# Optimization experiments

Hardware: AMD Instinct MI355X
Metric: run time of the kernel (lower is better)

The kernel has to match this reference:

```python
import jax, jax.numpy as jnp
import numpy as np


def setup_inputs() -> dict:
    key = jax.random.key(0)
    k1, k2, k3 = jax.random.split(key, 3)
    N, D, E = 4096, 1024, 8  # tokens, d_model, path_num (experts)
    x = jax.random.normal(k1, (N, D), dtype=jnp.float32)
    score = jax.random.uniform(k2, (N, E), dtype=jnp.float32)
    hot_mask = jax.random.randint(k3, (N, E), 0, 2).astype(jnp.int32)
    tag = jnp.arange(N, dtype=jnp.int32).reshape(N, 1)
    return {"x": x, "score": score, "hot_mask": hot_mask, "tag": tag}


def reference(x, score, hot_mask, tag):
    # Per-expert gather dispatch with score scaling (route_logic='1d', transform=True).
    # Torch version produces variable-length per-expert flows; here each expert's
    # output is packed into a fixed capacity of N slots (selected tokens first,
    # in original order, matching torch.nonzero ordering), zero-padded beyond count.
    N, D = x.shape
    E = hot_mask.shape[1]
    mask = hot_mask > 0  # [N, E] multi-hot routing mask
    pos = jnp.arange(N)

    def dispatch(mask_e, score_e):
        # stable partition: selected tokens get their index, others index+N
        order = jnp.argsort(jnp.where(mask_e, pos, pos + N))  # [N]
        count = mask_e.sum()
        valid = pos < count  # [N] first `count` slots hold real tokens
        data = x * score_e[:, None]  # transform: scale by routing score
        out_data = jnp.where(valid[:, None], data[order], 0.0)  # [N, D]
        out_tag = jnp.where(valid[:, None], tag[order], 0)      # [N, 1]
        return out_data, out_tag, count

    out_data, out_tags, counts = jax.vmap(dispatch, in_axes=(1, 1))(mask, score)
    # out_data: [E, N, D], out_tags: [E, N, 1], counts: [E]
    return out_data, out_tags, counts
```

## Files before the change

kernel.cpp:

```cpp
#include <hip/hip_runtime.h>

#define N_TOK 4096
#define DMODEL 1024
#define NEXP 8
#define BT 256
#define TPB 16

__global__ __launch_bounds__(BT) void build(
        const int* __restrict__ hot_mask,
        int* __restrict__ perm,
        float* __restrict__ out_tags,
        float* __restrict__ out_cnts) {
    const int e = blockIdx.x;
    const int t = threadIdx.x;
    const int base = t * TPB;

    unsigned int bits = 0;
    int s = 0;
#pragma unroll
    for (int j = 0; j < TPB; ++j) {
        int m = (hot_mask[(size_t)(base + j) * NEXP + e] > 0) ? 1 : 0;
        bits |= (unsigned int)m << j;
        s += m;
    }

    __shared__ int sm[BT];
    sm[t] = s;
    __syncthreads();
    for (int off = 1; off < BT; off <<= 1) {
        int v = (t >= off) ? sm[t - off] : 0;
        __syncthreads();
        sm[t] += v;
        __syncthreads();
    }
    const int cnt = sm[BT - 1];
    int run = (t == 0) ? 0 : sm[t - 1];

#pragma unroll
    for (int j = 0; j < TPB; ++j) {
        if ((bits >> j) & 1u) {
            const int slot = run++;
            perm[e * N_TOK + slot] = base + j;
            out_tags[e * N_TOK + slot] = (float)(base + j);
        }
    }
    for (int slot = cnt + t; slot < N_TOK; slot += BT) {
        perm[e * N_TOK + slot] = -1;
        out_tags[e * N_TOK + slot] = 0.0f;
    }
    if (t == 0) out_cnts[e] = (float)cnt;
}

__global__ __launch_bounds__(256) void gather_f32(
        const float* __restrict__ x,
        const float* __restrict__ score,
        const int* __restrict__ perm,
        float* __restrict__ out_data)
{
    const int blk = blockIdx.x;
    const int t = threadIdx.x;
    const int n = perm[blk];
    float4* orow = reinterpret_cast<float4*>(out_data + (size_t)blk * DMODEL) + t;

    if (n >= 0) {
        const int e = blk >> 12;
        const int nn = n & (N_TOK - 1);
        const float sc = score[nn * NEXP + e];
        float4 v = reinterpret_cast<const float4*>(x + (size_t)nn * DMODEL)[t];
        v.x *= sc; v.y *= sc; v.z *= sc; v.w *= sc;
        *orow = v;
    } else {
        *orow = make_float4(0.f, 0.f, 0.f, 0.f);
    }
}

extern "C" void kernel_launch(void* const* d_in, const int* in_sizes, int n_in,
                              void* d_out, int out_size, void* d_ws, size_t ws_size,
                              hipStream_t stream) {
    const float* x        = (const float*)d_in[0];
    const float* score    = (const float*)d_in[1];
    const int*   hot_mask = (const int*)d_in[2];

    float* out      = (float*)d_out;
    float* out_data = out;
    float* out_tags = out + (size_t)NEXP * N_TOK * DMODEL;
    float* out_cnts = out_tags + (size_t)NEXP * N_TOK;

    int* perm = (int*)d_ws;

    build<<<NEXP, BT, 0, stream>>>(hot_mask, perm, out_tags, out_cnts);
    gather_f32<<<NEXP * N_TOK, 256, 0, stream>>>(x, score, perm, out_data);
}
```

Measured before the change: 38.63 us.

## Process 16 rows per gather block with nontemporal stores and shared perm/score

The gather kernel now uses 1024-thread blocks that each handle 16 output rows, with the permutation indices and routing scores loaded once into shared memory. Output is written with nontemporal stores so the 128 MB of output does not pollute the cache, and the build kernel moves to 512 threads with 8 tokens each. This cuts the block count and the per-row overhead of separate perm/score loads. It adds a block-wide barrier and a larger block size, which can reduce scheduling flexibility.

Result: faster. 36.38 us (-5.8%).

```diff
diff --git a/kernel.cpp b/kernel.cpp
--- a/kernel.cpp
+++ b/kernel.cpp
@@ -3,8 +3,11 @@
 #define N_TOK 4096
 #define DMODEL 1024
 #define NEXP 8
-#define BT 256
-#define TPB 16
+#define BT 512
+#define TPB 8
+#define RPB 16
+
+typedef float vfloat4 __attribute__((ext_vector_type(4)));
 
 __global__ __launch_bounds__(BT) void build(
         const int* __restrict__ hot_mask,
@@ -51,26 +54,43 @@
     if (t == 0) out_cnts[e] = (float)cnt;
 }
 
-__global__ __launch_bounds__(256) void gather_f32(
+__global__ __launch_bounds__(1024) void gather_f32(
         const float* __restrict__ x,
         const float* __restrict__ score,
         const int* __restrict__ perm,
         float* __restrict__ out_data)
 {
-    const int blk = blockIdx.x;
-    const int t = threadIdx.x;
-    const int n = perm[blk];
-    float4* orow = reinterpret_cast<float4*>(out_data + (size_t)blk * DMODEL) + t;
+    const int row0 = blockIdx.x * RPB;
+    const int e = row0 >> 12;
+    const int tid = threadIdx.x;
 
-    if (n >= 0) {
-        const int e = blk >> 12;
-        const int nn = n & (N_TOK - 1);
-        const float sc = score[nn * NEXP + e];
-        float4 v = reinterpret_cast<const float4*>(x + (size_t)nn * DMODEL)[t];
-        v.x *= sc; v.y *= sc; v.z *= sc; v.w *= sc;
-        *orow = v;
-    } else {
-        *orow = make_float4(0.f, 0.f, 0.f, 0.f);
+    __shared__ int   s_n[RPB];
+    __shared__ float s_sc[RPB];
+    if (tid < RPB) {
+        const int n = perm[row0 + tid];
+        s_n[tid] = n;
+        s_sc[tid] = (n >= 0) ? score[(n & (N_TOK - 1)) * NEXP + e] : 0.0f;
+    }
+    __syncthreads();
+
+    const int t  = tid & 255;
+    const int r0 = tid >> 8;
+#pragma unroll
+    for (int i = 0; i < 4; ++i) {
+        const int r = r0 + 4 * i;
+        const int n = s_n[r];
+        vfloat4* orow = reinterpret_cast<vfloat4*>(
+            out_data + (size_t)(row0 + r) * DMODEL) + t;
+        vfloat4 v;
+        if (n >= 0) {
+            v = reinterpret_cast<const vfloat4*>(
+                    x + (size_t)(n & (N_TOK - 1)) * DMODEL)[t];
+            const float sc = s_sc[r];
+            v *= sc;
+        } else {
+            v = (vfloat4)(0.f);
+        }
+        __builtin_nontemporal_store(v, orow);
     }
 }
 
@@ -89,5 +109,5 @@
     int* perm = (int*)d_ws;
 
     build<<<NEXP, BT, 0, stream>>>(hot_mask, perm, out_tags, out_cnts);
-    gather_f32<<<NEXP * N_TOK, 256, 0, stream>>>(x, score, perm, out_data);
+    gather_f32<<<(NEXP * N_TOK) / RPB, 1024, 0, stream>>>(x, score, perm, out_data);
 }
```

## Replace per-slot gather with per-token scatter plus separate zero-padding blocks

Applied to the files above, without the earlier changes.

Build now emits an inverse mapping (token,expert)->slot and integer counts, using 512 threads with 8 tokens each. The data kernel reads each x row once and scatters scaled copies to every selected expert with nontemporal stores. Separate blocks zero-fill only the padding rows, 16 rows per block. This cuts x reads from eight to one per token, but the scatter writes are non-contiguous across experts and the kernel is now more complex.

Measured after the change: 36.77 us. 1.05x faster.

```diff
diff --git a/kernel.cpp b/kernel.cpp
--- a/kernel.cpp
+++ b/kernel.cpp
@@ -3,12 +3,16 @@
 #define N_TOK 4096
 #define DMODEL 1024
 #define NEXP 8
-#define BT 256
-#define TPB 16
+#define BT 512
+#define TPB 8
+#define PRPB 16
+
+typedef float vfloat4 __attribute__((ext_vector_type(4)));
 
 __global__ __launch_bounds__(BT) void build(
         const int* __restrict__ hot_mask,
-        int* __restrict__ perm,
+        int* __restrict__ islot,
+        int* __restrict__ cnt_i32,
         float* __restrict__ out_tags,
         float* __restrict__ out_cnts) {
     const int e = blockIdx.x;
@@ -38,39 +42,59 @@
 
 #pragma unroll
     for (int j = 0; j < TPB; ++j) {
+        const int tok = base + j;
+        int sl = -1;
         if ((bits >> j) & 1u) {
-            const int slot = run++;
-            perm[e * N_TOK + slot] = base + j;
-            out_tags[e * N_TOK + slot] = (float)(base + j);
+            sl = run++;
+            out_tags[e * N_TOK + sl] = (float)tok;
         }
+        islot[tok * NEXP + e] = sl;
     }
-    for (int slot = cnt + t; slot < N_TOK; slot += BT) {
-        perm[e * N_TOK + slot] = -1;
+    for (int slot = cnt + t; slot < N_TOK; slot += BT)
         out_tags[e * N_TOK + slot] = 0.0f;
+    if (t == 0) {
+        out_cnts[e] = (float)cnt;
+        cnt_i32[e] = cnt;
     }
-    if (t == 0) out_cnts[e] = (float)cnt;
 }
 
-__global__ __launch_bounds__(256) void gather_f32(
+__global__ __launch_bounds__(256) void scatter_and_pad(
         const float* __restrict__ x,
         const float* __restrict__ score,
-        const int* __restrict__ perm,
+        const int* __restrict__ islot,
+        const int* __restrict__ cnt_i32,
         float* __restrict__ out_data)
 {
-    const int blk = blockIdx.x;
+    const int b = blockIdx.x;
     const int t = threadIdx.x;
-    const int n = perm[blk];
-    float4* orow = reinterpret_cast<float4*>(out_data + (size_t)blk * DMODEL) + t;
 
-    if (n >= 0) {
-        const int e = blk >> 12;
-        const int nn = n & (N_TOK - 1);
-        const float sc = score[nn * NEXP + e];
-        float4 v = reinterpret_cast<const float4*>(x + (size_t)nn * DMODEL)[t];
-        v.x *= sc; v.y *= sc; v.z *= sc; v.w *= sc;
-        *orow = v;
+    if (b < N_TOK) {
+        const int n = b;
+        const vfloat4 v = reinterpret_cast<const vfloat4*>(
+                              x + (size_t)n * DMODEL)[t];
+#pragma unroll
+        for (int e = 0; e < NEXP; ++e) {
+            const int sl = islot[n * NEXP + e];
+            if (sl >= 0) {
+                vfloat4 w = v * score[n * NEXP + e];
+                __builtin_nontemporal_store(
+                    w, reinterpret_cast<vfloat4*>(
+                           out_data + ((size_t)e * N_TOK + sl) * DMODEL) + t);
+            }
+        }
     } else {
-        *orow = make_float4(0.f, 0.f, 0.f, 0.f);
+        const int row0  = (b - N_TOK) * PRPB;
+        const int e     = row0 >> 12;
+        const int slot0 = row0 & (N_TOK - 1);
+        const int cnt   = cnt_i32[e];
+        if (slot0 + PRPB <= cnt) return;
+        const vfloat4 z = (vfloat4)(0.f);
+        for (int r = 0; r < PRPB; ++r) {
+            if (slot0 + r < cnt) continue;
+            __builtin_nontemporal_store(
+                z, reinterpret_cast<vfloat4*>(
+                       out_data + (size_t)(row0 + r) * DMODEL) + t);
+        }
     }
 }
 
@@ -86,8 +110,11 @@
     float* out_tags = out + (size_t)NEXP * N_TOK * DMODEL;
     float* out_cnts = out_tags + (size_t)NEXP * N_TOK;
 
-    int* perm = (int*)d_ws;
+    int* islot   = (int*)d_ws;
+    int* cnt_i32 = islot + N_TOK * NEXP;
 
-    build<<<NEXP, BT, 0, stream>>>(hot_mask, perm, out_tags, out_cnts);
-    gather_f32<<<NEXP * N_TOK, 256, 0, stream>>>(x, score, perm, out_data);
+    const int npad = (NEXP * N_TOK) / PRPB;
+    build<<<NEXP, BT, 0, stream>>>(hot_mask, islot, cnt_i32, out_tags, out_cnts);
+    scatter_and_pad<<<N_TOK + npad, 256, 0, stream>>>(
+        x, score, islot, cnt_i32, out_data);
 }
```
